# Optimization experiments

Measured on AMD Instinct MI355X. Metric: run time of the kernel, lower is better.

## Reference

```python
import jax, jax.numpy as jnp
import numpy as np

D_MODEL = 1024
NUM_HEADS = 16
HEAD_DIM = D_MODEL // NUM_HEADS
THETA = 10000.0
BATCH, SEQ = 2, 2048


def rope(x, token_positions):
    # x: [b, h, s, d]; token_positions: [s]
    d = x.shape[-1]
    freqs = 1.0 / THETA ** (jnp.arange(0, d, 2, dtype=jnp.float32)[: d // 2] / d)
    ang = token_positions.astype(jnp.float32)[:, None] * freqs[None, :]  # [s, d/2]
    cos, sin = jnp.cos(ang), jnp.sin(ang)
    xr = x.reshape(*x.shape[:-1], d // 2, 2)
    x_even, x_odd = xr[..., 0], xr[..., 1]
    out_even = x_even * cos - x_odd * sin
    out_odd = x_even * sin + x_odd * cos
    return jnp.stack([out_even, out_odd], axis=-1).reshape(x.shape)


def setup_inputs() -> dict:
    key = jax.random.key(0)
    ks = jax.random.split(key, 5)
    std = np.sqrt(2.0 / (D_MODEL + D_MODEL))
    mk = lambda k: (jax.random.truncated_normal(k, -3.0, 3.0, (D_MODEL, D_MODEL), jnp.float32) * std)
    return {
        "x": jax.random.normal(ks[0], (BATCH, SEQ, D_MODEL), jnp.float32),
        "Wq": mk(ks[1]),
        "Wk": mk(ks[2]),
        "Wv": mk(ks[3]),
        "Wo": mk(ks[4]),
        "casual_mask": jnp.tril(jnp.ones((SEQ, SEQ), dtype=bool)),
        "token_positions": jnp.arange(SEQ, dtype=jnp.int32),
    }


def reference(x, Wq, Wk, Wv, Wo, casual_mask, token_positions):
    b, s, _ = x.shape
    split = lambda t: t.reshape(b, s, NUM_HEADS, HEAD_DIM).transpose(0, 2, 1, 3)
    q = split(x @ Wq.T)  # [b, h, s, d]
    k = split(x @ Wk.T)
    v = split(x @ Wv.T)
    q = rope(q, token_positions)
    k = rope(k, token_positions)
    scores = jnp.einsum("bhqd,bhkd->bhqk", q, k) / np.sqrt(HEAD_DIM)
    scores = jnp.where(casual_mask, scores, -jnp.inf)
    probs = jax.nn.softmax(scores, axis=-1)
    out = jnp.einsum("bhqk,bhkd->bhqd", probs, v)
    out = out.transpose(0, 2, 1, 3).reshape(b, s, D_MODEL)
    return out @ Wo.T
```

## Files before the change

### kernel.cpp

```cpp
#include <hip/hip_runtime.h>
#include <hip/hip_bf16.h>

#define SEQ_LEN 2048
#define NBATCH 2
#define DM 1024
#define NH 16
#define HD 64
#define NR (NBATCH * SEQ_LEN)
#define NQKV (3 * DM)
#define LDQK 2048

typedef __attribute__((ext_vector_type(8))) short bf16x8;
typedef __attribute__((ext_vector_type(4))) float f32x4;

__device__ __forceinline__ short f2b(float f) {
    __hip_bfloat16 h = __float2bfloat16(f);
    return *reinterpret_cast<short*>(&h);
}
__device__ __forceinline__ float b2f(short s) {
    union { unsigned u; float f; } x;
    x.u = ((unsigned)(unsigned short)s) << 16;
    return x.f;
}

__device__ __forceinline__ void gload_lds16(const void* g, void* l) {
    __builtin_amdgcn_global_load_lds(
        (const __attribute__((address_space(1))) unsigned int*)g,
        (__attribute__((address_space(3))) unsigned int*)l, 16, 0, 0);
}

__global__ __launch_bounds__(256) void cvt_all(
    const float* __restrict__ x,  const float* __restrict__ wq,
    const float* __restrict__ wk, const float* __restrict__ wv,
    const float* __restrict__ wo,
    __hip_bfloat16* __restrict__ xb, __hip_bfloat16* __restrict__ wqkvb,
    __hip_bfloat16* __restrict__ wob) {
    int id = blockIdx.x;
    const float* src; __hip_bfloat16* dst;
    if (id < 4096) { src = x + (size_t)id * 1024; dst = xb + (size_t)id * 1024; }
    else {
        int k = id - 4096, seg = k >> 10;
        size_t off = (size_t)(k & 1023) * 1024;
        if      (seg == 0) { src = wq + off; dst = wqkvb + off; }
        else if (seg == 1) { src = wk + off; dst = wqkvb + (1u << 20) + off; }
        else if (seg == 2) { src = wv + off; dst = wqkvb + (2u << 20) + off; }
        else               { src = wo + off; dst = wob + off; }
    }
    int i = threadIdx.x * 4;
    float4 v = *(const float4*)(src + i);
    dst[i + 0] = __float2bfloat16(v.x);
    dst[i + 1] = __float2bfloat16(v.y);
    dst[i + 2] = __float2bfloat16(v.z);
    dst[i + 3] = __float2bfloat16(v.w);
}

__device__ __forceinline__ void store_c(float* p, float v) { *p = v; }
__device__ __forceinline__ void store_c(__hip_bfloat16* p, float v) {
    *p = __float2bfloat16(v);
}

template <typename CT, bool FUSED>
__global__ __launch_bounds__(256) void gemm128(
    const __hip_bfloat16* __restrict__ A,
    const __hip_bfloat16* __restrict__ B,
    CT* __restrict__ C, int K, int ldc,
    __hip_bfloat16* __restrict__ Vtg) {
    __shared__ __hip_bfloat16 As[128 * 32];
    __shared__ __hip_bfloat16 Bs[128 * 32];
    const int t    = threadIdx.x;
    const int wave = t >> 6;
    const int lane = t & 63;
    const int quad = lane >> 4;
    const int l16  = lane & 15;
    const int wy = wave >> 1, wx = wave & 1;
    const int m0 = blockIdx.x * 128, n0 = blockIdx.y * 128;

    const int r0 = wave * 32 + (lane >> 2);
    const int c0 = (lane & 3) * 8;
    const __hip_bfloat16* Ag0 = A + (size_t)(m0 + r0) * K + c0;
    const __hip_bfloat16* Ag1 = Ag0 + (size_t)16 * K;
    const __hip_bfloat16* Bg0 = B + (size_t)(n0 + r0) * K + c0;
    const __hip_bfloat16* Bg1 = Bg0 + (size_t)16 * K;
    __hip_bfloat16* lA0 = &As[r0 * 32 + c0];
    __hip_bfloat16* lA1 = &As[(r0 + 16) * 32 + c0];
    __hip_bfloat16* lB0 = &Bs[r0 * 32 + c0];
    __hip_bfloat16* lB1 = &Bs[(r0 + 16) * 32 + c0];

    f32x4 acc[4][4];
#pragma unroll
    for (int i = 0; i < 4; i++)
#pragma unroll
        for (int j = 0; j < 4; j++) acc[i][j] = (f32x4){0.f, 0.f, 0.f, 0.f};

    for (int k0 = 0; k0 < K; k0 += 32) {
        __syncthreads();
        gload_lds16(Ag0 + k0, lA0);
        gload_lds16(Ag1 + k0, lA1);
        gload_lds16(Bg0 + k0, lB0);
        gload_lds16(Bg1 + k0, lB1);
        __syncthreads();

        bf16x8 af[4], bfr[4];
#pragma unroll
        for (int rb = 0; rb < 4; rb++)
            af[rb] = *(const bf16x8*)&As[(wy * 64 + rb * 16 + l16) * 32 + quad * 8];
#pragma unroll
        for (int cb = 0; cb < 4; cb++)
            bfr[cb] = *(const bf16x8*)&Bs[(wx * 64 + cb * 16 + l16) * 32 + quad * 8];
#pragma unroll
        for (int rb = 0; rb < 4; rb++)
#pragma unroll
            for (int cb = 0; cb < 4; cb++)
                acc[rb][cb] = __builtin_amdgcn_mfma_f32_16x16x32_bf16(
                    af[rb], bfr[cb], acc[rb][cb], 0, 0, 0);
    }

    if (!FUSED || blockIdx.y < 16) {
#pragma unroll
        for (int rb = 0; rb < 4; rb++)
#pragma unroll
            for (int r = 0; r < 4; r++) {
                size_t ro = (size_t)(m0 + wy * 64 + rb * 16 + quad * 4 + r) * ldc;
#pragma unroll
                for (int cb = 0; cb < 4; cb++)
                    store_c(&C[ro + n0 + wx * 64 + cb * 16 + l16], acc[rb][cb][r]);
            }
    } else {
#pragma unroll
        for (int rb = 0; rb < 4; rb++) {
            int row0 = m0 + wy * 64 + rb * 16 + quad * 4;
            int bb = row0 >> 11, ss = row0 & (SEQ_LEN - 1);
#pragma unroll
            for (int cb = 0; cb < 4; cb++) {
                int vcol = n0 + wx * 64 + cb * 16 + l16 - 2048;
                int hh = vcol >> 6, dd = vcol & 63;
                ushort4 u;
                u.x = (unsigned short)f2b(acc[rb][cb][0]);
                u.y = (unsigned short)f2b(acc[rb][cb][1]);
                u.z = (unsigned short)f2b(acc[rb][cb][2]);
                u.w = (unsigned short)f2b(acc[rb][cb][3]);
                *(ushort4*)(Vtg + ((size_t)(bb * NH + hh) * HD + dd) * SEQ_LEN + ss) = u;
            }
        }
    }
}

__global__ __launch_bounds__(256) void rope_kernel(
    __hip_bfloat16* __restrict__ QK, const int* __restrict__ pos) {
    int idx = blockIdx.x * 256 + threadIdx.x;
    int row  = idx >> 8;
    int tcol = idx & 255;
    int col0 = tcol * 8;
    int head = col0 >> 6;
    int i0   = (col0 & 63) >> 1;
    float p  = (float)pos[row & (SEQ_LEN - 1)];
    float scale = (head < NH) ? 0.125f : 1.0f;
    __hip_bfloat16* ptr = QK + (size_t)row * LDQK + col0;
    bf16x8 v = *(const bf16x8*)ptr;
    bf16x8 o;
#pragma unroll
    for (int k = 0; k < 4; k++) {
        float fr = __expf(-(float)(2 * (i0 + k)) * (9.210340371976184f / 64.0f));
        float ang = p * fr;
        float sn = sinf(ang), cs = cosf(ang);
        float e  = b2f(v[2 * k]);
        float od = b2f(v[2 * k + 1]);
        o[2 * k]     = f2b((e * cs - od * sn) * scale);
        o[2 * k + 1] = f2b((e * sn + od * cs) * scale);
    }
    *(bf16x8*)ptr = o;
}

__global__ __launch_bounds__(512) void attn_kernel(
    const __hip_bfloat16* __restrict__ QK,
    const __hip_bfloat16* __restrict__ Vtg,
    __hip_bfloat16* __restrict__ O) {
    __shared__ short Ps[256][72];

    const int t    = threadIdx.x;
    const int wave = t >> 6;
    const int team = wave >> 2;
    const int w4   = wave & 3;
    const int lane = t & 63;
    const int quad = lane >> 4;
    const int l16  = lane & 15;
    const int pairIdx = blockIdx.x;
    const int h    = blockIdx.y;
    const int b    = blockIdx.z;

    const int qt   = team == 0 ? pairIdx : 15 - pairIdx;
    const int row0 = qt * 128 + w4 * 32;

    bf16x8 qf[2][2];
#pragma unroll
    for (int g = 0; g < 2; g++) {
        const __hip_bfloat16* qp =
            QK + (size_t)(b * SEQ_LEN + row0 + g * 16 + l16) * LDQK + h * HD + quad * 8;
        qf[g][0] = *(const bf16x8*)qp;
        qf[g][1] = *(const bf16x8*)(qp + 32);
    }

    f32x4 o[2][4];
    float l_p[2][4];
#pragma unroll
    for (int g = 0; g < 2; g++)
#pragma unroll
        for (int r = 0; r < 4; r++) {
            o[g][r] = (f32x4){0.f, 0.f, 0.f, 0.f};
            l_p[g][r] = 0.f;
        }

    const __hip_bfloat16* kbase = QK + (size_t)(b * SEQ_LEN) * LDQK + DM + h * HD;
    const __hip_bfloat16* vbase = Vtg + (size_t)((b * NH + h) * HD) * SEQ_LEN;

    const int ktmax = (row0 + 31) >> 6;
    for (int kt = 0; kt <= ktmax; kt++) {
        bf16x8 kf[4][2], vf[4][2];
#pragma unroll
        for (int kb = 0; kb < 4; kb++) {
            const __hip_bfloat16* kp =
                kbase + (size_t)(kt * 64 + kb * 16 + l16) * LDQK + quad * 8;
            kf[kb][0] = *(const bf16x8*)kp;
            kf[kb][1] = *(const bf16x8*)(kp + 32);
        }
#pragma unroll
        for (int db = 0; db < 4; db++) {
            const __hip_bfloat16* vp =
                vbase + (size_t)(db * 16 + l16) * SEQ_LEN + kt * 64 + quad * 8;
            vf[db][0] = *(const bf16x8*)vp;
            vf[db][1] = *(const bf16x8*)(vp + 32);
        }

        f32x4 s[2][4];
#pragma unroll
        for (int g = 0; g < 2; g++)
#pragma unroll
            for (int kb = 0; kb < 4; kb++) {
                f32x4 z = {0.f, 0.f, 0.f, 0.f};
                z = __builtin_amdgcn_mfma_f32_16x16x32_bf16(qf[g][0], kf[kb][0], z, 0, 0, 0);
                z = __builtin_amdgcn_mfma_f32_16x16x32_bf16(qf[g][1], kf[kb][1], z, 0, 0, 0);
                s[g][kb] = z;
            }

        if (kt == ktmax) {
#pragma unroll
            for (int g = 0; g < 2; g++)
#pragma unroll
                for (int kb = 0; kb < 4; kb++) {
                    int key = kt * 64 + kb * 16 + l16;
#pragma unroll
                    for (int r = 0; r < 4; r++) {
                        int rowg = row0 + g * 16 + quad * 4 + r;
                        if (key > rowg) s[g][kb][r] = -1e30f;
                    }
                }
        }

#pragma unroll
        for (int g = 0; g < 2; g++)
#pragma unroll
            for (int r = 0; r < 4; r++) {
                float p0 = __expf(s[g][0][r]);
                float p1 = __expf(s[g][1][r]);
                float p2 = __expf(s[g][2][r]);
                float p3 = __expf(s[g][3][r]);
                l_p[g][r] += (p0 + p1) + (p2 + p3);
                int prow = wave * 32 + g * 16 + quad * 4 + r;
                Ps[prow][ 0 + l16] = f2b(p0);
                Ps[prow][16 + l16] = f2b(p1);
                Ps[prow][32 + l16] = f2b(p2);
                Ps[prow][48 + l16] = f2b(p3);
            }

#pragma unroll
        for (int g = 0; g < 2; g++) {
            bf16x8 pf0 = *(const bf16x8*)&Ps[wave * 32 + g * 16 + l16][quad * 8];
            bf16x8 pf1 = *(const bf16x8*)&Ps[wave * 32 + g * 16 + l16][32 + quad * 8];
#pragma unroll
            for (int db = 0; db < 4; db++) {
                o[g][db] = __builtin_amdgcn_mfma_f32_16x16x32_bf16(pf0, vf[db][0], o[g][db], 0, 0, 0);
                o[g][db] = __builtin_amdgcn_mfma_f32_16x16x32_bf16(pf1, vf[db][1], o[g][db], 0, 0, 0);
            }
        }
    }

#pragma unroll
    for (int g = 0; g < 2; g++)
#pragma unroll
        for (int r = 0; r < 4; r++) {
            float rs = l_p[g][r];
            rs += __shfl_xor(rs, 1);
            rs += __shfl_xor(rs, 2);
            rs += __shfl_xor(rs, 4);
            rs += __shfl_xor(rs, 8);
            float inv = 1.0f / rs;
            size_t ro = (size_t)(b * SEQ_LEN + row0 + g * 16 + quad * 4 + r) * DM + h * HD;
            O[ro +  0 + l16] = __float2bfloat16(o[g][0][r] * inv);
            O[ro + 16 + l16] = __float2bfloat16(o[g][1][r] * inv);
            O[ro + 32 + l16] = __float2bfloat16(o[g][2][r] * inv);
            O[ro + 48 + l16] = __float2bfloat16(o[g][3][r] * inv);
        }
}

extern "C" void kernel_launch(void* const* d_in, const int* in_sizes, int n_in,
                              void* d_out, int out_size, void* d_ws, size_t ws_size,
                              hipStream_t stream) {
    const float* x  = (const float*)d_in[0];
    const float* Wq = (const float*)d_in[1];
    const float* Wk = (const float*)d_in[2];
    const float* Wv = (const float*)d_in[3];
    const float* Wo = (const float*)d_in[4];
    const int* pos = (const int*)d_in[6];
    float* out = (float*)d_out;

    char* w = (char*)d_ws;
    const size_t MiB = 1024 * 1024;
    __hip_bfloat16* xb    = (__hip_bfloat16*)(w + 0 * MiB);
    __hip_bfloat16* Ab    = (__hip_bfloat16*)(w + 0 * MiB);
    __hip_bfloat16* Wqkvb = (__hip_bfloat16*)(w + 8 * MiB);
    __hip_bfloat16* Wob   = (__hip_bfloat16*)(w + 14 * MiB);
    __hip_bfloat16* QKb   = (__hip_bfloat16*)(w + 16 * MiB);
    __hip_bfloat16* Vtg   = (__hip_bfloat16*)(w + 32 * MiB);

    cvt_all<<<8192, 256, 0, stream>>>(x, Wq, Wk, Wv, Wo, xb, Wqkvb, Wob);

    gemm128<__hip_bfloat16, true><<<dim3(NR / 128, NQKV / 128), 256, 0, stream>>>(
        xb, Wqkvb, QKb, DM, LDQK, Vtg);

    rope_kernel<<<NR * LDQK / 8 / 256, 256, 0, stream>>>(QKb, pos);

    attn_kernel<<<dim3(8, NH, NBATCH), 512, 0, stream>>>(QKb, Vtg, Ab);

    gemm128<float, false><<<dim3(NR / 128, DM / 128), 256, 0, stream>>>(
        Ab, Wob, out, DM, DM, nullptr);
}
```

Before: 233.3 us.

## Double-buffer K loads in attention and split V transpose into its own kernel

The attention loop now prefetches the next K tile into a second register set while computing the current tile. The attention kernel also gets an occupancy hint of two blocks per SM. The P matrix is written to shared memory as packed short4 stores using a permuted key order. V is no longer transposed in the QKV GEMM epilogue. The GEMM writes a plain QKV buffer, and a new LDS-tiled transpose kernel produces V^T in the matching permuted key order. This aims to hide global load latency and cut LDS store instructions, at the cost of an extra kernel launch, an extra pass over V, and more register pressure from the doubled K fragments.

Measured after the change: 235.0 us. No clear change (+0.8%).

```diff
diff --git a/kernel.cpp b/kernel.cpp
--- a/kernel.cpp
+++ b/kernel.cpp
@@ -8,7 +8,6 @@
 #define HD 64
 #define NR (NBATCH * SEQ_LEN)
 #define NQKV (3 * DM)
-#define LDQK 2048
 
 typedef __attribute__((ext_vector_type(8))) short bf16x8;
 typedef __attribute__((ext_vector_type(4))) float f32x4;
@@ -59,12 +58,11 @@
     *p = __float2bfloat16(v);
 }
 
-template <typename CT, bool FUSED>
+template <typename CT>
 __global__ __launch_bounds__(256) void gemm128(
     const __hip_bfloat16* __restrict__ A,
     const __hip_bfloat16* __restrict__ B,
-    CT* __restrict__ C, int K, int ldc,
-    __hip_bfloat16* __restrict__ Vtg) {
+    CT* __restrict__ C, int K, int ldc) {
     __shared__ __hip_bfloat16 As[128 * 32];
     __shared__ __hip_bfloat16 Bs[128 * 32];
     const int t    = threadIdx.x;
@@ -115,38 +113,19 @@
                     af[rb], bfr[cb], acc[rb][cb], 0, 0, 0);
     }
 
-    if (!FUSED || blockIdx.y < 16) {
-#pragma unroll
-        for (int rb = 0; rb < 4; rb++)
-#pragma unroll
-            for (int r = 0; r < 4; r++) {
-                size_t ro = (size_t)(m0 + wy * 64 + rb * 16 + quad * 4 + r) * ldc;
-#pragma unroll
-                for (int cb = 0; cb < 4; cb++)
-                    store_c(&C[ro + n0 + wx * 64 + cb * 16 + l16], acc[rb][cb][r]);
-            }
-    } else {
-#pragma unroll
-        for (int rb = 0; rb < 4; rb++) {
-            int row0 = m0 + wy * 64 + rb * 16 + quad * 4;
-            int bb = row0 >> 11, ss = row0 & (SEQ_LEN - 1);
-#pragma unroll
-            for (int cb = 0; cb < 4; cb++) {
-                int vcol = n0 + wx * 64 + cb * 16 + l16 - 2048;
-                int hh = vcol >> 6, dd = vcol & 63;
-                ushort4 u;
-                u.x = (unsigned short)f2b(acc[rb][cb][0]);
-                u.y = (unsigned short)f2b(acc[rb][cb][1]);
-                u.z = (unsigned short)f2b(acc[rb][cb][2]);
-                u.w = (unsigned short)f2b(acc[rb][cb][3]);
-                *(ushort4*)(Vtg + ((size_t)(bb * NH + hh) * HD + dd) * SEQ_LEN + ss) = u;
-            }
-        }
-    }
+#pragma unroll
+    for (int rb = 0; rb < 4; rb++)
+#pragma unroll
+        for (int r = 0; r < 4; r++) {
+            size_t ro = (size_t)(m0 + wy * 64 + rb * 16 + quad * 4 + r) * ldc;
+#pragma unroll
+            for (int cb = 0; cb < 4; cb++)
+                store_c(&C[ro + n0 + wx * 64 + cb * 16 + l16], acc[rb][cb][r]);
+        }
 }
 
 __global__ __launch_bounds__(256) void rope_kernel(
-    __hip_bfloat16* __restrict__ QK, const int* __restrict__ pos) {
+    __hip_bfloat16* __restrict__ QKV, const int* __restrict__ pos) {
     int idx = blockIdx.x * 256 + threadIdx.x;
     int row  = idx >> 8;
     int tcol = idx & 255;
@@ -155,7 +134,7 @@
     int i0   = (col0 & 63) >> 1;
     float p  = (float)pos[row & (SEQ_LEN - 1)];
     float scale = (head < NH) ? 0.125f : 1.0f;
-    __hip_bfloat16* ptr = QK + (size_t)row * LDQK + col0;
+    __hip_bfloat16* ptr = QKV + (size_t)row * NQKV + col0;
     bf16x8 v = *(const bf16x8*)ptr;
     bf16x8 o;
 #pragma unroll
@@ -171,7 +150,37 @@
     *(bf16x8*)ptr = o;
 }
 
-__global__ __launch_bounds__(512) void attn_kernel(
+__global__ __launch_bounds__(256) void transpose_v_kernel(
+    const __hip_bfloat16* __restrict__ QKV, __hip_bfloat16* __restrict__ Vtg) {
+    __shared__ short Ts[64][72];
+    const int t  = threadIdx.x;
+    const int r0 = blockIdx.x * 64;
+    const int h  = blockIdx.y;
+    const int b  = r0 >> 11;
+    const int sb = r0 & (SEQ_LEN - 1);
+
+    const int lr  = t >> 3;
+    const int lcq = (t & 7) * 8;
+#pragma unroll
+    for (int pass = 0; pass < 2; pass++) {
+        int rr = lr + pass * 32;
+        int pc = 4 * (rr & 15) + (rr >> 4);
+        bf16x8 v = *(const bf16x8*)(QKV + (size_t)(r0 + rr) * NQKV + 2 * DM + h * HD + lcq);
+#pragma unroll
+        for (int e = 0; e < 8; e++) Ts[lcq + e][pc] = v[e];
+    }
+    __syncthreads();
+    const int dr = t >> 3;
+    const int sc = (t & 7) * 8;
+#pragma unroll
+    for (int pass = 0; pass < 2; pass++) {
+        int dd = dr + pass * 32;
+        bf16x8 v = *(const bf16x8*)&Ts[dd][sc];
+        *(bf16x8*)(Vtg + ((size_t)(b * NH + h) * HD + dd) * SEQ_LEN + sb + sc) = v;
+    }
+}
+
+__global__ __launch_bounds__(512, 2) void attn_kernel(
     const __hip_bfloat16* __restrict__ QK,
     const __hip_bfloat16* __restrict__ Vtg,
     __hip_bfloat16* __restrict__ O) {
@@ -195,7 +204,7 @@
 #pragma unroll
     for (int g = 0; g < 2; g++) {
         const __hip_bfloat16* qp =
-            QK + (size_t)(b * SEQ_LEN + row0 + g * 16 + l16) * LDQK + h * HD + quad * 8;
+            QK + (size_t)(b * SEQ_LEN + row0 + g * 16 + l16) * NQKV + h * HD + quad * 8;
         qf[g][0] = *(const bf16x8*)qp;
         qf[g][1] = *(const bf16x8*)(qp + 32);
     }
@@ -210,19 +219,22 @@
             l_p[g][r] = 0.f;
         }
 
-    const __hip_bfloat16* kbase = QK + (size_t)(b * SEQ_LEN) * LDQK + DM + h * HD;
+    const __hip_bfloat16* kbase = QK + (size_t)(b * SEQ_LEN) * NQKV + DM + h * HD;
     const __hip_bfloat16* vbase = Vtg + (size_t)((b * NH + h) * HD) * SEQ_LEN;
-
     const int ktmax = (row0 + 31) >> 6;
-    for (int kt = 0; kt <= ktmax; kt++) {
-        bf16x8 kf[4][2], vf[4][2];
+
+    auto load_k = [&](bf16x8 kf[4][2], int kt) {
 #pragma unroll
         for (int kb = 0; kb < 4; kb++) {
             const __hip_bfloat16* kp =
-                kbase + (size_t)(kt * 64 + kb * 16 + l16) * LDQK + quad * 8;
+                kbase + (size_t)(kt * 64 + kb * 16 + l16) * NQKV + quad * 8;
             kf[kb][0] = *(const bf16x8*)kp;
             kf[kb][1] = *(const bf16x8*)(kp + 32);
         }
+    };
+
+    auto step = [&](bf16x8 kf[4][2], int kt) {
+        bf16x8 vf[4][2];
 #pragma unroll
         for (int db = 0; db < 4; db++) {
             const __hip_bfloat16* vp =
@@ -266,10 +278,9 @@
                 float p3 = __expf(s[g][3][r]);
                 l_p[g][r] += (p0 + p1) + (p2 + p3);
                 int prow = wave * 32 + g * 16 + quad * 4 + r;
-                Ps[prow][ 0 + l16] = f2b(p0);
-                Ps[prow][16 + l16] = f2b(p1);
-                Ps[prow][32 + l16] = f2b(p2);
-                Ps[prow][48 + l16] = f2b(p3);
+                short4 pk;
+                pk.x = f2b(p0); pk.y = f2b(p1); pk.z = f2b(p2); pk.w = f2b(p3);
+                *(short4*)&Ps[prow][4 * l16] = pk;
             }
 
 #pragma unroll
@@ -282,6 +293,20 @@
                 o[g][db] = __builtin_amdgcn_mfma_f32_16x16x32_bf16(pf1, vf[db][1], o[g][db], 0, 0, 0);
             }
         }
+    };
+
+    bf16x8 kfA[4][2], kfB[4][2];
+    load_k(kfA, 0);
+    int kt = 0;
+    while (true) {
+        if (kt < ktmax) load_k(kfB, kt + 1);
+        step(kfA, kt);
+        kt++;
+        if (kt > ktmax) break;
+        if (kt < ktmax) load_k(kfA, kt + 1);
+        step(kfB, kt);
+        kt++;
+        if (kt > ktmax) break;
     }
 
 #pragma unroll
@@ -319,18 +344,20 @@
     __hip_bfloat16* Ab    = (__hip_bfloat16*)(w + 0 * MiB);
     __hip_bfloat16* Wqkvb = (__hip_bfloat16*)(w + 8 * MiB);
     __hip_bfloat16* Wob   = (__hip_bfloat16*)(w + 14 * MiB);
-    __hip_bfloat16* QKb   = (__hip_bfloat16*)(w + 16 * MiB);
-    __hip_bfloat16* Vtg   = (__hip_bfloat16*)(w + 32 * MiB);
+    __hip_bfloat16* QKVb  = (__hip_bfloat16*)(w + 16 * MiB);
+    __hip_bfloat16* Vtg   = (__hip_bfloat16*)(w + 40 * MiB);
 
     cvt_all<<<8192, 256, 0, stream>>>(x, Wq, Wk, Wv, Wo, xb, Wqkvb, Wob);
 
-    gemm128<__hip_bfloat16, true><<<dim3(NR / 128, NQKV / 128), 256, 0, stream>>>(
-        xb, Wqkvb, QKb, DM, LDQK, Vtg);
-
-    rope_kernel<<<NR * LDQK / 8 / 256, 256, 0, stream>>>(QKb, pos);
-
-    attn_kernel<<<dim3(8, NH, NBATCH), 512, 0, stream>>>(QKb, Vtg, Ab);
-
-    gemm128<float, false><<<dim3(NR / 128, DM / 128), 256, 0, stream>>>(
-        Ab, Wob, out, DM, DM, nullptr);
-}
+    gemm128<__hip_bfloat16><<<dim3(NR / 128, NQKV / 128), 256, 0, stream>>>(
+        xb, Wqkvb, QKVb, DM, NQKV);
+
+    rope_kernel<<<NR * 2048 / 8 / 256, 256, 0, stream>>>(QKVb, pos);
+
+    transpose_v_kernel<<<dim3(NR / 64, NH), 256, 0, stream>>>(QKVb, Vtg);
+
+    attn_kernel<<<dim3(8, NH, NBATCH), 512, 0, stream>>>(QKVb, Vtg, Ab);
+
+    gemm128<float><<<dim3(NR / 128, DM / 128), 256, 0, stream>>>(
+        Ab, Wob, out, DM, DM);
+}
```
